# Kernel optimization log

Measured on AMD Instinct MI355X. Metric: run time of the kernel, lower is better.

Reference implementation:

```python
import jax, jax.numpy as jnp
import numpy as np

B, T, E = 64, 512, 512          # batch, seq_len, embedding_size
H2 = 512                        # per-direction hidden = hidden_size // 2
V = 32000                       # vocab
PAD = 0                         # padding_idx


def _lstm_scan(x_tbe, mask_tb, Wih, Whh, bih, bhh):
    """Masked LSTMCell loop over time (PyTorch gate order i,f,g,o).
    x_tbe: (T,B,E) time-major, mask_tb: (T,B). Returns (out (T,B,H), hT, cT)."""
    Bn = x_tbe.shape[1]
    Hn = Whh.shape[1]
    h0 = jnp.zeros((Bn, Hn), x_tbe.dtype)
    c0 = jnp.zeros((Bn, Hn), x_tbe.dtype)

    def step(carry, xm):
        h, c = carry
        x, m = xm
        gates = x @ Wih.T + bih + h @ Whh.T + bhh  # (B, 4H)
        i, f, g, o = jnp.split(gates, 4, axis=-1)
        i = jax.nn.sigmoid(i)
        f = jax.nn.sigmoid(f)
        o = jax.nn.sigmoid(o)
        g = jnp.tanh(g)
        c_new = f * c + i * g
        h_new = o * jnp.tanh(c_new)
        m = m[:, None]
        # masked update: padded steps carry state through unchanged
        h_new = h_new * m + h * (1.0 - m)
        c_new = c_new * m + c * (1.0 - m)
        return (h_new, c_new), h_new

    (hT, cT), out = jax.lax.scan(step, (h0, c0), (x_tbe, mask_tb))
    return out, hT, cT


def _encoder(inputs, lengths, emb_table, Wih_f, Whh_f, bih_f, bhh_f,
             Wih_b, Whh_b, bih_b, bhh_b):
    table = emb_table.at[PAD].set(0.0)      # padding_idx row is zero
    embeds = table[inputs]                  # (B,T,E); dropout p=0 -> no-op
    mask = (jnp.arange(T)[None, :] < lengths[:, None]).astype(embeds.dtype)  # (B,T)
    x = embeds.transpose(1, 0, 2)           # (T,B,E) time-major
    m = mask.T                              # (T,B)
    out_f, ht_f, ct_f = _lstm_scan(x, m, Wih_f, Whh_f, bih_f, bhh_f)
    out_b, ht_b, ct_b = _lstm_scan(x[::-1], m[::-1], Wih_b, Whh_b, bih_b, bhh_b)
    output = jnp.concatenate([out_f, out_b[::-1]], axis=2)   # (T,B,2*H2)
    ht = jnp.concatenate([ht_f, ht_b], axis=1)               # (B,2*H2) (squeezed num_layers=1)
    ct = jnp.concatenate([ct_f, ct_b], axis=1)
    return output.transpose(1, 0, 2), ht, ct, mask           # output (B,T,H)


def setup_inputs() -> dict:
    key = jax.random.key(0)
    ks = jax.random.split(key, 12)
    s_e = 1.0 / np.sqrt(E)
    s_h = 1.0 / np.sqrt(H2)
    inp = {
        "inputs": jax.random.randint(ks[0], (B, T), 0, V, dtype=jnp.int64 if jax.config.jax_enable_x64 else jnp.int32),
        "lengths": jax.random.randint(ks[1], (B,), 1, T + 1, dtype=jnp.int64 if jax.config.jax_enable_x64 else jnp.int32),
        "emb_table": jax.random.normal(ks[2], (V, E), jnp.float32) * 0.02,
        "Wih_f": jax.random.normal(ks[3], (4 * H2, E), jnp.float32) * s_e,
        "Whh_f": jax.random.normal(ks[4], (4 * H2, H2), jnp.float32) * s_h,
        "bih_f": jax.random.normal(ks[5], (4 * H2,), jnp.float32) * s_h,
        "bhh_f": jax.random.normal(ks[6], (4 * H2,), jnp.float32) * s_h,
        "Wih_b": jax.random.normal(ks[7], (4 * H2, E), jnp.float32) * s_e,
        "Whh_b": jax.random.normal(ks[8], (4 * H2, H2), jnp.float32) * s_h,
        "bih_b": jax.random.normal(ks[9], (4 * H2,), jnp.float32) * s_h,
        "bhh_b": jax.random.normal(ks[10], (4 * H2,), jnp.float32) * s_h,
    }
    return inp


def reference(inputs, lengths, emb_table, Wih_f, Whh_f, bih_f, bhh_f,
              Wih_b, Whh_b, bih_b, bhh_b):
    return _encoder(inputs, lengths, emb_table, Wih_f, Whh_f, bih_f, bhh_f,
                    Wih_b, Whh_b, bih_b, bhh_b)
```

## Files before the change

kernel.cpp:

```cpp
#include <hip/hip_runtime.h>


#define Bn 64
#define Tn 512
#define NWG 64
#define TC 32
#define NCH 16

#define OUT_HT  33554432u
#define OUT_CT  33619968u
#define OUT_MSK 33685504u

#define WS_WCAT 0ull
#define WS_GXB  8388608ull
#define WS_REC  25165824ull
#define WS_HST  25690112ull
#define WS_CST  25952256ull

typedef __bf16 v8bf __attribute__((ext_vector_type(8)));
typedef float  v4f  __attribute__((ext_vector_type(4)));
typedef unsigned v4u __attribute__((ext_vector_type(4)));
typedef unsigned v2u __attribute__((ext_vector_type(2)));

__device__ __forceinline__ unsigned short f2bf(float f) {
    unsigned u = __float_as_uint(f);
    u = (u + 0x7FFFu + ((u >> 16) & 1u)) >> 16;
    return (unsigned short)u;
}

__device__ __forceinline__ void bf2x(unsigned u, float& lo, float& hi) {
    lo = __uint_as_float(u << 16);
    hi = __uint_as_float(u & 0xffff0000u);
}

__device__ __forceinline__ v8bf ldfrag(const unsigned short* p) {
    return *reinterpret_cast<const v8bf*>(p);
}

__device__ __forceinline__ v4u ld_co16(const void* p) {
    v4u r;
    asm volatile("global_load_dwordx4 %0, %1, off sc0 sc1" : "=v"(r) : "v"(p));
    return r;
}

__device__ __forceinline__ float fsig(float x) {
    return 1.0f / (1.0f + __expf(-x));
}
__device__ __forceinline__ float ftanh(float x) {
    x = fminf(fmaxf(x, -15.0f), 15.0f);
    float e = __expf(2.0f * x);
    return (e - 1.0f) / (e + 1.0f);
}


__global__ void k_weights(const float* __restrict__ Wih_f, const float* __restrict__ Whh_f,
                          const float* __restrict__ Wih_b, const float* __restrict__ Whh_b,
                          unsigned short* __restrict__ Wcat) {
    int idx = blockIdx.x * 256 + threadIdx.x;
    if (idx >= 2 * 2048 * 256) return;
    int k4 = idx & 255;
    int n  = (idx >> 8) & 2047;
    int d  = idx >> 19;
    int k  = k4 * 4;
    const float* src;
    if (k < 512) src = (d ? Wih_b : Wih_f) + (size_t)n * 512 + k;
    else         src = (d ? Whh_b : Whh_f) + (size_t)n * 512 + (k - 512);
    float4 v = *(const float4*)src;
    unsigned short o[4] = { f2bf(v.x), f2bf(v.y), f2bf(v.z), f2bf(v.w) };
    *(ushort4*)(Wcat + (size_t)idx * 4) = *(const ushort4*)o;
}

__global__ void k_zero(unsigned char* __restrict__ recb,
                       float* __restrict__ hstate, float* __restrict__ cstate) {
    int i = blockIdx.x * 256 + threadIdx.x;
    if (i < 32768) { v4u z = {0,0,0,0}; ((v4u*)recb)[i] = z; }
    if (i < 65536) { hstate[i] = 0.0f; cstate[i] = 0.0f; }
}

__global__ void k_mask(const int* __restrict__ lengths, float* __restrict__ mask_out) {
    int i = blockIdx.x * 256 + threadIdx.x;
    if (i >= Bn * Tn) return;
    int b = i >> 9, t = i & 511;
    mask_out[i] = (t < lengths[b]) ? 1.0f : 0.0f;
}


__global__ __launch_bounds__(256) void k_gx(
    const int* __restrict__ inputs,
    const float* __restrict__ table,
    const unsigned short* __restrict__ Wcat,
    const float* __restrict__ bih_f, const float* __restrict__ bhh_f,
    const float* __restrict__ bih_b, const float* __restrict__ bhh_b,
    unsigned short* __restrict__ gxb, int s0)
{
    __shared__ unsigned short Bs[128 * 512];
    const int bi   = blockIdx.x;
    const int nt   = bi >> 4;
    const int d    = (bi >> 3) & 1;
    const int slg  = bi & 7;
    const int n0   = nt * 128;
    const int tid  = threadIdx.x;
    const int lane = tid & 63, wave = tid >> 6;
    const int l15  = lane & 15, kq = lane >> 4;

    const unsigned short* Wd = Wcat + (size_t)d * (2048 * 1024);

    #pragma unroll
    for (int i = 0; i < 32; ++i) {
        int w = i * 256 + tid;
        int r = w >> 6, c = w & 63;
        v4u tmp = *(const v4u*)(Wd + (size_t)(n0 + r) * 1024 + c * 8);
        *(v4u*)&Bs[r * 512 + ((c ^ (r & 7)) * 8)] = tmp;
    }

    const float* bih = d ? bih_b : bih_f;
    const float* bhh = d ? bhh_b : bhh_f;
    float bv[8];
    #pragma unroll
    for (int n2 = 0; n2 < 8; ++n2) {
        int n = n0 + n2 * 16 + l15;
        bv[n2] = bih[n] + bhh[n];
    }
    __syncthreads();

    const int ab   = wave * 16 + l15;
    const int brow = wave * 16 + kq * 4;

    #pragma unroll 1
    for (int q = 0; q < 4; ++q) {
        const int sl = slg * 4 + q;
        const int s  = s0 + sl;
        const int t  = d ? (511 - s) : s;
        const int tok = inputs[ab * 512 + t];

        v8bf af[16];
        if (tok != 0) {
            const float* tr = table + (size_t)tok * 512 + kq * 8;
            #pragma unroll
            for (int ks = 0; ks < 16; ++ks) {
                float4 v0 = *(const float4*)(tr + ks * 32);
                float4 v1 = *(const float4*)(tr + ks * 32 + 4);
                unsigned short o[8] = { f2bf(v0.x), f2bf(v0.y), f2bf(v0.z), f2bf(v0.w),
                                        f2bf(v1.x), f2bf(v1.y), f2bf(v1.z), f2bf(v1.w) };
                af[ks] = *(const v8bf*)o;
            }
        } else {
            v4u z = {0u, 0u, 0u, 0u};
            #pragma unroll
            for (int ks = 0; ks < 16; ++ks) af[ks] = __builtin_bit_cast(v8bf, z);
        }

        unsigned short* gbase = gxb + ((size_t)(d * TC + sl) * 64) * 2048;
        #pragma unroll
        for (int n2 = 0; n2 < 8; ++n2) {
            v4f acc = {0, 0, 0, 0};
            const int rb = n2 * 16 + l15;
            const unsigned short* bbp = Bs + rb * 512;
            const int sw = rb & 7;
            #pragma unroll
            for (int ks = 0; ks < 16; ++ks) {
                v8bf bf = *(const v8bf*)&bbp[((ks * 4 + kq) ^ sw) * 8];
                acc = __builtin_amdgcn_mfma_f32_16x16x32_bf16(af[ks], bf, acc, 0, 0, 0);
            }
            const int n = n0 + n2 * 16 + l15;
            #pragma unroll
            for (int qq = 0; qq < 4; ++qq)
                gbase[(size_t)(brow + qq) * 2048 + n] = f2bf(acc[qq] + bv[n2]);
        }
    }
}


__global__ __launch_bounds__(256, 1) void lstm_recur(
    const unsigned short* __restrict__ Wcat,
    unsigned char* __restrict__ recb,
    const unsigned short* __restrict__ gxb,
    const int* __restrict__ lengths,
    float* __restrict__ out,
    float* __restrict__ hstate,
    float* __restrict__ cstate,
    int s0)
{
    const int wg   = blockIdx.x;
    const int dir  = wg >> 5;
    const int hc0  = (wg & 31) * 16;
    const int tid  = threadIdx.x;
    const int lane = tid & 63;
    const int wave = tid >> 6;
    const int wm   = wave >> 1, wn = wave & 1;
    const int l15  = lane & 15, kq = lane >> 4;
    const int eb   = tid >> 2, ejg = tid & 3;

    __shared__ unsigned short hA[64 * 512];
    __shared__ float gLds[64][65];
    __shared__ float hS[64][17];
    __shared__ float cS[64][17];
    __shared__ int   lenS[64];

    {
        const size_t so = (size_t)dir * (64 * 512) + (size_t)eb * 512 + hc0 + ejg * 4;
        v4f hv = *(const v4f*)(hstate + so);
        v4f cv = *(const v4f*)(cstate + so);
        #pragma unroll
        for (int jj = 0; jj < 4; ++jj) { hS[eb][ejg * 4 + jj] = hv[jj]; cS[eb][ejg * 4 + jj] = cv[jj]; }
        if (tid < 64) lenS[tid] = lengths[tid];
    }

    const unsigned short* Wd = Wcat + (size_t)dir * (2048 * 1024);
    const int rowA0 = 32 * wm + l15, rowA1 = rowA0 + 16;
    const int n0 = (2 * wn + 0) * 512 + hc0 + l15;
    const int n1 = (2 * wn + 1) * 512 + hc0 + l15;
    const unsigned short* pB0 = Wd + (size_t)n0 * 1024 + kq * 8;
    const unsigned short* pB1 = Wd + (size_t)n1 * 1024 + kq * 8;

    v8bf whB0[16], whB1[16];
    #pragma unroll
    for (int ks = 0; ks < 16; ++ks) {
        whB0[ks] = ldfrag(pB0 + (16 + ks) * 32);
        whB1[ks] = ldfrag(pB1 + (16 + ks) * 32);
    }

    const unsigned short* lA0 = hA + rowA0 * 512;
    const unsigned short* lA1 = hA + rowA1 * 512;
    const int swA0 = (rowA0 & 7) << 3, swA1 = (rowA1 & 7) << 3;

    unsigned char* recD = recb + (size_t)dir * 262144;

    __syncthreads();

    for (int sl = 0; sl < TC; ++sl) {
        const int s = s0 + sl;
        const int t = dir ? (511 - s) : s;
        const unsigned want = (unsigned)s;

        v2u gw0, gw1, gw2, gw3;
        {
            const unsigned short* g = gxb + ((size_t)(dir * TC + sl) * 64 + eb) * 2048 + hc0 + ejg * 4;
            gw0 = *(const v2u*)(g);
            gw1 = *(const v2u*)(g + 512);
            gw2 = *(const v2u*)(g + 1024);
            gw3 = *(const v2u*)(g + 1536);
        }

        unsigned char* rp = recD + (size_t)(s & 1) * 131072;
        #pragma unroll
        for (int grp = 0; grp < 4; ++grp) {
            v4u r[8];
            #pragma unroll
            for (int i = 0; i < 8; ++i)
                r[i] = ld_co16(rp + (size_t)((grp * 8 + i) * 256 + tid) * 16);
            asm volatile("s_waitcnt vmcnt(0)" ::: "memory");
            __builtin_amdgcn_sched_barrier(0);
            unsigned stale = 0u;
            #pragma unroll
            for (int i = 0; i < 8; ++i) {
                int idx = (grp * 8 + i) * 256 + tid;
                if (r[i][3] == want) {
                    int b = idx >> 7, j4 = idx & 127;
                    v2u hv = { r[i][0], r[i][1] };
                    *(v2u*)&hA[b * 512 + ((j4 * 4) ^ ((b & 7) << 3))] = hv;
                } else {
                    stale |= (1u << i);
                }
            }
            while (__any(stale != 0u)) {
                v4u q[8];
                #pragma unroll
                for (int i = 0; i < 8; ++i)
                    q[i] = ld_co16(rp + (size_t)((grp * 8 + i) * 256 + tid) * 16);
                asm volatile("s_waitcnt vmcnt(0)" ::: "memory");
                __builtin_amdgcn_sched_barrier(0);
                #pragma unroll
                for (int i = 0; i < 8; ++i) {
                    if ((stale & (1u << i)) && q[i][3] == want) {
                        int idx = (grp * 8 + i) * 256 + tid;
                        int b = idx >> 7, j4 = idx & 127;
                        v2u hv = { q[i][0], q[i][1] };
                        *(v2u*)&hA[b * 512 + ((j4 * 4) ^ ((b & 7) << 3))] = hv;
                        stale &= ~(1u << i);
                    }
                }
            }
        }
        __syncthreads();

        v4f a00 = {0,0,0,0}, a01 = {0,0,0,0}, a10 = {0,0,0,0}, a11 = {0,0,0,0};
        #pragma unroll
        for (int ks = 0; ks < 16; ++ks) {
            v8bf fa0 = *(const v8bf*)&lA0[(kq * 8 + ks * 32) ^ swA0];
            v8bf fa1 = *(const v8bf*)&lA1[(kq * 8 + ks * 32) ^ swA1];
            a00 = __builtin_amdgcn_mfma_f32_16x16x32_bf16(fa0, whB0[ks], a00, 0, 0, 0);
            a01 = __builtin_amdgcn_mfma_f32_16x16x32_bf16(fa0, whB1[ks], a01, 0, 0, 0);
            a10 = __builtin_amdgcn_mfma_f32_16x16x32_bf16(fa1, whB0[ks], a10, 0, 0, 0);
            a11 = __builtin_amdgcn_mfma_f32_16x16x32_bf16(fa1, whB1[ks], a11, 0, 0, 0);
        }

        {
            int c0 = 32 * wn + l15;
            int rr = 32 * wm + kq * 4;
            #pragma unroll
            for (int q = 0; q < 4; ++q) {
                gLds[rr + q][c0     ] = a00[q];
                gLds[rr + q][c0 + 16] = a01[q];
                gLds[rr + 16 + q][c0     ] = a10[q];
                gLds[rr + 16 + q][c0 + 16] = a11[q];
            }
        }
        __syncthreads();

        {
            const int b = eb, jg = ejg;
            const int msk = (t < lenS[b]);
            float gxi[4], gxf[4], gxg[4], gxo[4];
            bf2x(gw0[0], gxi[0], gxi[1]); bf2x(gw0[1], gxi[2], gxi[3]);
            bf2x(gw1[0], gxf[0], gxf[1]); bf2x(gw1[1], gxf[2], gxf[3]);
            bf2x(gw2[0], gxg[0], gxg[1]); bf2x(gw2[1], gxg[2], gxg[3]);
            bf2x(gw3[0], gxo[0], gxo[1]); bf2x(gw3[1], gxo[2], gxo[3]);
            float hn[4], cn[4];
            #pragma unroll
            for (int jj = 0; jj < 4; ++jj) {
                int j = jg * 4 + jj;
                float gi = gLds[b][j]      + gxi[jj];
                float gf = gLds[b][16 + j] + gxf[jj];
                float gg = gLds[b][32 + j] + gxg[jj];
                float go = gLds[b][48 + j] + gxo[jj];
                float i_ = fsig(gi), f_ = fsig(gf), o_ = fsig(go), g_ = ftanh(gg);
                float c_old = cS[b][j], h_old = hS[b][j];
                float c_new = fmaf(f_, c_old, i_ * g_);
                float h_new = o_ * ftanh(c_new);
                if (!msk) { c_new = c_old; h_new = h_old; }
                cS[b][j] = c_new;
                hS[b][j] = h_new;
                hn[jj] = h_new; cn[jj] = c_new;
            }
            if (s < 511) {
                unsigned short q0 = f2bf(hn[0]), q1 = f2bf(hn[1]), q2 = f2bf(hn[2]), q3 = f2bf(hn[3]);
                v4u pk = { (unsigned)q0 | ((unsigned)q1 << 16),
                           (unsigned)q2 | ((unsigned)q3 << 16),
                           0u, (unsigned)(s + 1) };
                int idxp = b * 128 + (wg & 31) * 4 + jg;
                unsigned char* dst = recD + (size_t)((s + 1) & 1) * 131072 + (size_t)idxp * 16;
                asm volatile("global_store_dwordx4 %0, %1, off sc0 sc1" :: "v"(dst), "v"(pk) : "memory");
            }
            v4f ov = {hn[0], hn[1], hn[2], hn[3]};
            *(v4f*)&out[((size_t)b * 512 + t) * 1024 + (size_t)dir * 512 + hc0 + jg * 4] = ov;
            if (s == 511) {
                v4f cv2 = {cn[0], cn[1], cn[2], cn[3]};
                *(v4f*)&out[OUT_HT + (size_t)b * 1024 + dir * 512 + hc0 + jg * 4] = ov;
                *(v4f*)&out[OUT_CT + (size_t)b * 1024 + dir * 512 + hc0 + jg * 4] = cv2;
            }
        }
        __syncthreads();
    }

    {
        float hv[4], cv[4];
        #pragma unroll
        for (int jj = 0; jj < 4; ++jj) { hv[jj] = hS[eb][ejg * 4 + jj]; cv[jj] = cS[eb][ejg * 4 + jj]; }
        const size_t so = (size_t)dir * (64 * 512) + (size_t)eb * 512 + hc0 + ejg * 4;
        *(v4f*)(hstate + so) = *(v4f*)hv;
        *(v4f*)(cstate + so) = *(v4f*)cv;
    }
}


extern "C" void kernel_launch(void* const* d_in, const int* in_sizes, int n_in,
                              void* d_out, int out_size, void* d_ws, size_t ws_size,
                              hipStream_t stream) {
    (void)in_sizes; (void)n_in; (void)out_size; (void)ws_size;

    const int*   inputs  = (const int*)d_in[0];
    const int*   lengths = (const int*)d_in[1];
    const float* table   = (const float*)d_in[2];
    const float* Wih_f   = (const float*)d_in[3];
    const float* Whh_f   = (const float*)d_in[4];
    const float* bih_f   = (const float*)d_in[5];
    const float* bhh_f   = (const float*)d_in[6];
    const float* Wih_b   = (const float*)d_in[7];
    const float* Whh_b   = (const float*)d_in[8];
    const float* bih_b   = (const float*)d_in[9];
    const float* bhh_b   = (const float*)d_in[10];
    float* out = (float*)d_out;

    char* w = (char*)d_ws;
    unsigned short* Wcat   = (unsigned short*)(w + WS_WCAT);
    unsigned short* gxb    = (unsigned short*)(w + WS_GXB);
    unsigned char*  recb   = (unsigned char*)(w + WS_REC);
    float*          hstate = (float*)(w + WS_HST);
    float*          cstate = (float*)(w + WS_CST);

    k_weights<<<4096, 256, 0, stream>>>(Wih_f, Whh_f, Wih_b, Whh_b, Wcat);
    k_zero<<<256, 256, 0, stream>>>(recb, hstate, cstate);
    k_mask<<<128, 256, 0, stream>>>(lengths, out + OUT_MSK);

    for (int ch = 0; ch < NCH; ++ch) {
        k_gx<<<256, 256, 0, stream>>>(inputs, table, Wcat,
                                      bih_f, bhh_f, bih_b, bhh_b, gxb, ch * TC);
        lstm_recur<<<NWG, 256, 0, stream>>>(Wcat, recb, gxb, lengths, out,
                                            hstate, cstate, ch * TC);
    }
}
```

Measured before the change: 4.262 ms.

## Overlap next chunk's input projection with current recurrence via fused kernel

Fuses the input-gate GEMM (k_gx) for the next time chunk into the recurrent kernel launch as extra workgroups, double-buffering the gx workspace. The 64 recurrence workgroups process chunk ch while 128 extra workgroups compute gx for chunk ch+1. This removes the serialized k_gx launches between recurrence chunks and fills idle CUs. The risk is that the extra blocks compete for memory bandwidth and L2 with the latency-sensitive recurrence, which spins on cross-workgroup flags. Co-residency of the 64 spinning blocks also matters, though they are launched first.

```diff
diff --git a/kernel.cpp b/kernel.cpp
--- a/kernel.cpp
+++ b/kernel.cpp
@@ -12,10 +12,11 @@
 #define OUT_MSK 33685504u
 
 #define WS_WCAT 0ull
-#define WS_GXB  8388608ull
-#define WS_REC  25165824ull
-#define WS_HST  25690112ull
-#define WS_CST  25952256ull
+#define WS_GX0  8388608ull
+#define WS_GX1  25165824ull
+#define WS_REC  41943040ull
+#define WS_HST  42467328ull
+#define WS_CST  42729472ull
 
 typedef __bf16 v8bf __attribute__((ext_vector_type(8)));
 typedef float  v4f  __attribute__((ext_vector_type(4)));
@@ -85,102 +86,146 @@
 }
 
 
+__device__ __forceinline__ void gx_unit(
+    unsigned short* __restrict__ Bs,
+    const int* __restrict__ inputs,
+    const float* __restrict__ table,
+    const unsigned short* __restrict__ Wcat,
+    const float* __restrict__ bih, const float* __restrict__ bhh,
+    unsigned short* __restrict__ gxw,
+    int d, int slg, int nt, int s0,
+    int tid)
+{
+    const int lane = tid & 63, wave = tid >> 6;
+    const int l15  = lane & 15, kq = lane >> 4;
+    const int n0   = nt * 128;
+
+    const unsigned short* Wd = Wcat + (size_t)d * (2048 * 1024);
+
+    #pragma unroll
+    for (int i = 0; i < 32; ++i) {
+        int w = i * 256 + tid;
+        int r = w >> 6, c = w & 63;
+        v4u tmp = *(const v4u*)(Wd + (size_t)(n0 + r) * 1024 + c * 8);
+        *(v4u*)&Bs[r * 512 + ((c ^ (r & 7)) * 8)] = tmp;
+    }
+
+    float bv[8];
+    #pragma unroll
+    for (int n2 = 0; n2 < 8; ++n2) {
+        int n = n0 + n2 * 16 + l15;
+        bv[n2] = bih[n] + bhh[n];
+    }
+    __syncthreads();
+
+    const int ab   = wave * 16 + l15;
+    const int brow = wave * 16 + kq * 4;
+
+    #pragma unroll 1
+    for (int q = 0; q < 4; ++q) {
+        const int sl = slg * 4 + q;
+        const int s  = s0 + sl;
+        const int t  = d ? (511 - s) : s;
+        const int tok = inputs[ab * 512 + t];
+
+        v8bf af[16];
+        if (tok != 0) {
+            const float* tr = table + (size_t)tok * 512 + kq * 8;
+            #pragma unroll
+            for (int ks = 0; ks < 16; ++ks) {
+                float4 v0 = *(const float4*)(tr + ks * 32);
+                float4 v1 = *(const float4*)(tr + ks * 32 + 4);
+                unsigned short o[8] = { f2bf(v0.x), f2bf(v0.y), f2bf(v0.z), f2bf(v0.w),
+                                        f2bf(v1.x), f2bf(v1.y), f2bf(v1.z), f2bf(v1.w) };
+                af[ks] = *(const v8bf*)o;
+            }
+        } else {
+            v4u z = {0u, 0u, 0u, 0u};
+            #pragma unroll
+            for (int ks = 0; ks < 16; ++ks) af[ks] = __builtin_bit_cast(v8bf, z);
+        }
+
+        unsigned short* gbase = gxw + ((size_t)(d * TC + sl) * 64) * 2048;
+        #pragma unroll
+        for (int n2 = 0; n2 < 8; ++n2) {
+            v4f acc = {0, 0, 0, 0};
+            const int rb = n2 * 16 + l15;
+            const unsigned short* bbp = Bs + rb * 512;
+            const int sw = rb & 7;
+            #pragma unroll
+            for (int ks = 0; ks < 16; ++ks) {
+                v8bf bf = *(const v8bf*)&bbp[((ks * 4 + kq) ^ sw) * 8];
+                acc = __builtin_amdgcn_mfma_f32_16x16x32_bf16(af[ks], bf, acc, 0, 0, 0);
+            }
+            const int n = n0 + n2 * 16 + l15;
+            #pragma unroll
+            for (int qq = 0; qq < 4; ++qq)
+                gbase[(size_t)(brow + qq) * 2048 + n] = f2bf(acc[qq] + bv[n2]);
+        }
+    }
+}
+
+
 __global__ __launch_bounds__(256) void k_gx(
     const int* __restrict__ inputs,
     const float* __restrict__ table,
     const unsigned short* __restrict__ Wcat,
     const float* __restrict__ bih_f, const float* __restrict__ bhh_f,
     const float* __restrict__ bih_b, const float* __restrict__ bhh_b,
-    unsigned short* __restrict__ gxb, int s0)
+    unsigned short* __restrict__ gxw, int s0)
 {
     __shared__ unsigned short Bs[128 * 512];
-    const int bi   = blockIdx.x;
-    const int nt   = bi >> 4;
-    const int d    = (bi >> 3) & 1;
-    const int slg  = bi & 7;
-    const int n0   = nt * 128;
-    const int tid  = threadIdx.x;
-    const int lane = tid & 63, wave = tid >> 6;
-    const int l15  = lane & 15, kq = lane >> 4;
-
-    const unsigned short* Wd = Wcat + (size_t)d * (2048 * 1024);
-
-    #pragma unroll
-    for (int i = 0; i < 32; ++i) {
-        int w = i * 256 + tid;
-        int r = w >> 6, c = w & 63;
-        v4u tmp = *(const v4u*)(Wd + (size_t)(n0 + r) * 1024 + c * 8);
-        *(v4u*)&Bs[r * 512 + ((c ^ (r & 7)) * 8)] = tmp;
-    }
-
-    const float* bih = d ? bih_b : bih_f;
-    const float* bhh = d ? bhh_b : bhh_f;
-    float bv[8];
-    #pragma unroll
-    for (int n2 = 0; n2 < 8; ++n2) {
-        int n = n0 + n2 * 16 + l15;
-        bv[n2] = bih[n] + bhh[n];
-    }
-    __syncthreads();
-
-    const int ab   = wave * 16 + l15;
-    const int brow = wave * 16 + kq * 4;
-
-    #pragma unroll 1
-    for (int q = 0; q < 4; ++q) {
-        const int sl = slg * 4 + q;
-        const int s  = s0 + sl;
-        const int t  = d ? (511 - s) : s;
-        const int tok = inputs[ab * 512 + t];
-
-        v8bf af[16];
-        if (tok != 0) {
-            const float* tr = table + (size_t)tok * 512 + kq * 8;
-            #pragma unroll
-            for (int ks = 0; ks < 16; ++ks) {
-                float4 v0 = *(const float4*)(tr + ks * 32);
-                float4 v1 = *(const float4*)(tr + ks * 32 + 4);
-                unsigned short o[8] = { f2bf(v0.x), f2bf(v0.y), f2bf(v0.z), f2bf(v0.w),
-                                        f2bf(v1.x), f2bf(v1.y), f2bf(v1.z), f2bf(v1.w) };
-                af[ks] = *(const v8bf*)o;
-            }
-        } else {
-            v4u z = {0u, 0u, 0u, 0u};
-            #pragma unroll
-            for (int ks = 0; ks < 16; ++ks) af[ks] = __builtin_bit_cast(v8bf, z);
-        }
-
-        unsigned short* gbase = gxb + ((size_t)(d * TC + sl) * 64) * 2048;
-        #pragma unroll
-        for (int n2 = 0; n2 < 8; ++n2) {
-            v4f acc = {0, 0, 0, 0};
-            const int rb = n2 * 16 + l15;
-            const unsigned short* bbp = Bs + rb * 512;
-            const int sw = rb & 7;
-            #pragma unroll
-            for (int ks = 0; ks < 16; ++ks) {
-                v8bf bf = *(const v8bf*)&bbp[((ks * 4 + kq) ^ sw) * 8];
-                acc = __builtin_amdgcn_mfma_f32_16x16x32_bf16(af[ks], bf, acc, 0, 0, 0);
-            }
-            const int n = n0 + n2 * 16 + l15;
-            #pragma unroll
-            for (int qq = 0; qq < 4; ++qq)
-                gbase[(size_t)(brow + qq) * 2048 + n] = f2bf(acc[qq] + bv[n2]);
-        }
-    }
-}
-
-
-__global__ __launch_bounds__(256, 1) void lstm_recur(
+    const int bi  = blockIdx.x;
+    const int nt  = bi >> 4;
+    const int d   = (bi >> 3) & 1;
+    const int slg = bi & 7;
+    gx_unit(Bs, inputs, table, Wcat,
+            d ? bih_b : bih_f, d ? bhh_b : bhh_f,
+            gxw, d, slg, nt, s0, threadIdx.x);
+}
+
+
+__global__ __launch_bounds__(256, 1) void fused(
     const unsigned short* __restrict__ Wcat,
     unsigned char* __restrict__ recb,
-    const unsigned short* __restrict__ gxb,
+    const unsigned short* __restrict__ gxb_rd,
+    unsigned short* __restrict__ gxb_wr,
+    const int* __restrict__ inputs,
+    const float* __restrict__ table,
+    const float* __restrict__ bih_f, const float* __restrict__ bhh_f,
+    const float* __restrict__ bih_b, const float* __restrict__ bhh_b,
     const int* __restrict__ lengths,
     float* __restrict__ out,
     float* __restrict__ hstate,
     float* __restrict__ cstate,
-    int s0)
+    int s0, int next_s0)
 {
+    __shared__ __align__(16) unsigned char smem[131072];
+
+    if (blockIdx.x >= 64) {
+        if (next_s0 < 0) return;
+        const int gxi = blockIdx.x - 64;
+        const int slg = gxi & 7;
+        const int np  = (gxi >> 3) & 7;
+        const int d   = gxi >> 6;
+        unsigned short* Bs = (unsigned short*)smem;
+        const float* bih = d ? bih_b : bih_f;
+        const float* bhh = d ? bhh_b : bhh_f;
+        #pragma unroll 1
+        for (int w2 = 0; w2 < 2; ++w2) {
+            gx_unit(Bs, inputs, table, Wcat, bih, bhh,
+                    gxb_wr, d, slg, np * 2 + w2, next_s0, threadIdx.x);
+            __syncthreads();
+        }
+        return;
+    }
+
+    unsigned short* hA = (unsigned short*)smem;
+    float (*gLds)[65]  = reinterpret_cast<float(*)[65]>(smem + 65536);
+    float (*hS)[17]    = reinterpret_cast<float(*)[17]>(smem + 82176);
+    float (*cS)[17]    = reinterpret_cast<float(*)[17]>(smem + 86528);
+    int* lenS          = reinterpret_cast<int*>(smem + 90880);
+
     const int wg   = blockIdx.x;
     const int dir  = wg >> 5;
     const int hc0  = (wg & 31) * 16;
@@ -191,12 +236,6 @@
     const int l15  = lane & 15, kq = lane >> 4;
     const int eb   = tid >> 2, ejg = tid & 3;
 
-    __shared__ unsigned short hA[64 * 512];
-    __shared__ float gLds[64][65];
-    __shared__ float hS[64][17];
-    __shared__ float cS[64][17];
-    __shared__ int   lenS[64];
-
     {
         const size_t so = (size_t)dir * (64 * 512) + (size_t)eb * 512 + hc0 + ejg * 4;
         v4f hv = *(const v4f*)(hstate + so);
@@ -235,7 +274,7 @@
 
         v2u gw0, gw1, gw2, gw3;
         {
-            const unsigned short* g = gxb + ((size_t)(dir * TC + sl) * 64 + eb) * 2048 + hc0 + ejg * 4;
+            const unsigned short* g = gxb_rd + ((size_t)(dir * TC + sl) * 64 + eb) * 2048 + hc0 + ejg * 4;
             gw0 = *(const v2u*)(g);
             gw1 = *(const v2u*)(g + 512);
             gw2 = *(const v2u*)(g + 1024);
@@ -384,19 +423,26 @@
 
     char* w = (char*)d_ws;
     unsigned short* Wcat   = (unsigned short*)(w + WS_WCAT);
-    unsigned short* gxb    = (unsigned short*)(w + WS_GXB);
+    unsigned short* gxb0   = (unsigned short*)(w + WS_GX0);
+    unsigned short* gxb1   = (unsigned short*)(w + WS_GX1);
     unsigned char*  recb   = (unsigned char*)(w + WS_REC);
     float*          hstate = (float*)(w + WS_HST);
     float*          cstate = (float*)(w + WS_CST);
+    unsigned short* gxb[2] = { gxb0, gxb1 };
 
     k_weights<<<4096, 256, 0, stream>>>(Wih_f, Whh_f, Wih_b, Whh_b, Wcat);
     k_zero<<<256, 256, 0, stream>>>(recb, hstate, cstate);
     k_mask<<<128, 256, 0, stream>>>(lengths, out + OUT_MSK);
 
+    k_gx<<<256, 256, 0, stream>>>(inputs, table, Wcat,
+                                  bih_f, bhh_f, bih_b, bhh_b, gxb0, 0);
+
     for (int ch = 0; ch < NCH; ++ch) {
-        k_gx<<<256, 256, 0, stream>>>(inputs, table, Wcat,
-                                      bih_f, bhh_f, bih_b, bhh_b, gxb, ch * TC);
-        lstm_recur<<<NWG, 256, 0, stream>>>(Wcat, recb, gxb, lengths, out,
-                                            hstate, cstate, ch * TC);
-    }
-}
+        const int next_s0 = (ch < NCH - 1) ? (ch + 1) * TC : -1;
+        fused<<<192, 256, 0, stream>>>(Wcat, recb, gxb[ch & 1], gxb[(ch + 1) & 1],
+                                       inputs, table,
+                                       bih_f, bhh_f, bih_b, bhh_b,
+                                       lengths, out, hstate, cstate,
+                                       ch * TC, next_s0);
+    }
+}
```

Measured after the change: 3.589 ms. 1.19x faster.
